# Performance work log

Measured on AMD Instinct MI355X. Metric: run time of the kernel, lower is better.

The kernel has to match this reference:

```python
import jax, jax.numpy as jnp
import numpy as np

H = 8          # n_heads
M = 16         # max_dist
U = 512        # n_units
DH = U // H    # d_head
EPS = 1e-3     # keras LayerNormalization default epsilon
NEG = -2.0**32 + 1.0


def _rel_table(pe, T):
    # pe: [2M+1, DH]; returns [T, T, DH] with rel[i, j] = pe[clip(j - i, -M, M) + M]
    i = jnp.arange(T)
    idx = jnp.clip(i[None, :] - i[:, None], -M, M) + M
    return pe[idx]


def _split_heads(x):
    # [B, T, U] -> [H*B, T, DH]  (head-major, matching tf.concat(tf.split(x, H, 2), 0))
    B, T, _ = x.shape
    return x.reshape(B, T, H, DH).transpose(2, 0, 1, 3).reshape(H * B, T, DH)


def _merge_heads(x, B):
    # [H*B, T, DH] -> [B, T, U]
    T = x.shape[1]
    return x.reshape(H, B, T, DH).transpose(1, 2, 0, 3).reshape(B, T, U)


def setup_inputs() -> dict:
    key = jax.random.key(0)
    ks = jax.random.split(key, 10)
    B, T = 8, 1024
    s = 1.0 / np.sqrt(U)
    inp = {
        'q': jax.random.normal(ks[0], (B, T, U), jnp.float32),
        'k': jax.random.normal(ks[1], (B, T, U), jnp.float32),
        'v': jax.random.normal(ks[2], (B, T, U), jnp.float32),
        'Wq': jax.random.normal(ks[3], (U, U), jnp.float32) * s,
        'bq': jnp.zeros((U,), jnp.float32),
        'Wk': jax.random.normal(ks[4], (U, U), jnp.float32) * s,
        'bk': jnp.zeros((U,), jnp.float32),
        'Wv': jax.random.normal(ks[5], (U, U), jnp.float32) * s,
        'bv': jnp.zeros((U,), jnp.float32),
        'Wo': jax.random.normal(ks[6], (U, U), jnp.float32) * s,
        'bo': jnp.zeros((U,), jnp.float32),
        'gamma': jnp.ones((U,), jnp.float32),
        'beta': jnp.zeros((U,), jnp.float32),
        'pe_k': jax.random.normal(ks[7], (2 * M + 1, DH), jnp.float32) * 0.05,
        'pe_v': jax.random.normal(ks[8], (2 * M + 1, DH), jnp.float32) * 0.05,
    }
    return inp


def reference(q, k, v, Wq, bq, Wk, bk, Wv, bv, Wo, bo, gamma, beta, pe_k, pe_v):
    B, T, _ = q.shape
    relu = jax.nn.relu
    q_emb = relu(q @ Wq + bq)
    k_emb = relu(k @ Wk + bk)
    v_emb = relu(v @ Wv + bv)
    qh = _split_heads(q_emb)   # [HB, T, DH]
    kh = _split_heads(k_emb)
    vh = _split_heads(v_emb)

    attn = jnp.einsum('btd,bsd->bts', qh, kh)
    rel_k = _rel_table(pe_k, T)                       # [T, T, DH]
    attn = attn + jnp.einsum('btd,tsd->bts', qh, rel_k)
    attn = attn / jnp.asarray(DH, attn.dtype) ** 0.5

    causal = jnp.tril(jnp.ones((T, T), jnp.bool_))
    attn = jnp.where(causal[None], attn, jnp.asarray(NEG, attn.dtype))
    w = jax.nn.softmax(attn, axis=-1)

    out = jnp.einsum('bts,bsd->btd', w, vh)
    rel_v = _rel_table(pe_v, T)
    out = out + jnp.einsum('bts,tsd->btd', w, rel_v)

    out = _merge_heads(out, B)                        # [B, T, U]
    out = relu(out @ Wo + bo)
    out = out + q

    mu = jnp.mean(out, axis=-1, keepdims=True)
    var = jnp.mean(jnp.square(out - mu), axis=-1, keepdims=True)
    return (out - mu) * jax.lax.rsqrt(var + EPS) * gamma + beta
```

## Files before the change

### kernel.cpp

```cpp
#include <hip/hip_runtime.h>
#include <hip/hip_bf16.h>

#define T_SEQ 1024
#define U_DIM 512
#define LN_EPS 1e-3f
#define LOG2E 1.44269504f

typedef float  f32x4  __attribute__((ext_vector_type(4)));
typedef short  bf16x8 __attribute__((ext_vector_type(8)));

__device__ __forceinline__ unsigned short f2bf(float f) {
    union { float f; unsigned u; } x; x.f = f;
    unsigned r = x.u + 0x7fffu + ((x.u >> 16) & 1u);
    return (unsigned short)(r >> 16);
}
__device__ __forceinline__ float b2f(short s) {
    union { unsigned u; float f; } x; x.u = ((unsigned)(unsigned short)s) << 16;
    return x.f;
}
__device__ __forceinline__ int packbf(float a, float b) {
    return (int)((unsigned)f2bf(a) | ((unsigned)f2bf(b) << 16));
}
__device__ __forceinline__ void async_copy16(void* lds, const void* g) {
    __builtin_amdgcn_global_load_lds((const __attribute__((address_space(1))) void*)g,
                                     (__attribute__((address_space(3))) void*)lds, 16, 0, 0);
}

#define WAITV(N) asm volatile("s_waitcnt vmcnt(" #N ")" ::: "memory")

__global__ __launch_bounds__(256) void prep_wt(
        const float* __restrict__ Wq, const float* __restrict__ Wk,
        const float* __restrict__ Wv, const float* __restrict__ Wo,
        short* __restrict__ wt) {
    __shared__ float Ws[64][65];
    const int bid = blockIdx.x, t = threadIdx.x;
    const int z = bid >> 6, tile = bid & 63;
    const float* W = (z == 0) ? Wq : (z == 1) ? Wk : (z == 2) ? Wv : Wo;
    short* Wt = wt + (size_t)z * 262144;
    const int k0 = (tile >> 3) * 64, n0 = (tile & 7) * 64;
    {
        const int kr = t >> 2, cs = (t & 3) * 16;
        const float4* src = (const float4*)(W + (size_t)(k0 + kr) * 512 + n0 + cs);
#pragma unroll
        for (int i = 0; i < 4; ++i) {
            float4 vv = src[i];
            Ws[kr][cs + 4 * i + 0] = vv.x;
            Ws[kr][cs + 4 * i + 1] = vv.y;
            Ws[kr][cs + 4 * i + 2] = vv.z;
            Ws[kr][cs + 4 * i + 3] = vv.w;
        }
    }
    __syncthreads();
    {
        const int nr = t >> 2, ks = (t & 3) * 16;
        int4 w0, w1;
        w0.x = packbf(Ws[ks + 0][nr], Ws[ks + 1][nr]);
        w0.y = packbf(Ws[ks + 2][nr], Ws[ks + 3][nr]);
        w0.z = packbf(Ws[ks + 4][nr], Ws[ks + 5][nr]);
        w0.w = packbf(Ws[ks + 6][nr], Ws[ks + 7][nr]);
        w1.x = packbf(Ws[ks + 8][nr], Ws[ks + 9][nr]);
        w1.y = packbf(Ws[ks + 10][nr], Ws[ks + 11][nr]);
        w1.z = packbf(Ws[ks + 12][nr], Ws[ks + 13][nr]);
        w1.w = packbf(Ws[ks + 14][nr], Ws[ks + 15][nr]);
        short* dst = Wt + (size_t)(n0 + nr) * 512 + k0 + ks;
        *(int4*)dst = w0;
        *(int4*)(dst + 8) = w1;
    }
}

__global__ __launch_bounds__(256) void gemm_cvt(
        const float* __restrict__ A0, const float* __restrict__ A1, const float* __restrict__ A2,
        const short* __restrict__ Wt0, const short* __restrict__ Wt1, const short* __restrict__ Wt2,
        const float* __restrict__ b0p, const float* __restrict__ b1p, const float* __restrict__ b2p,
        short* __restrict__ O0, short* __restrict__ O1, short* __restrict__ O2) {
    __shared__ short As[2 * 8192];
    __shared__ short Bs[2 * 8192];

    const int z = blockIdx.z;
    const float* Av = (z == 0) ? A0 : (z == 1) ? A1 : A2;
    const short* Wz = (z == 0) ? Wt0 : (z == 1) ? Wt1 : Wt2;
    const float* bz = (z == 0) ? b0p : (z == 1) ? b1p : b2p;
    short* Ov = (z == 0) ? O0 : (z == 1) ? O1 : O2;

    const int tid = threadIdx.x;
    const int m0 = blockIdx.x * 128, n0 = blockIdx.y * 128;
    const int w = tid >> 6, lane = tid & 63;
    const int n15 = lane & 15, g = lane >> 4;
    const int mh = w >> 1, nh = w & 1;
    const int lr = tid >> 4, c4 = tid & 15;

    f32x4 acc[4][4];
#pragma unroll
    for (int i = 0; i < 4; ++i)
#pragma unroll
        for (int j = 0; j < 4; ++j) acc[i][j] = (f32x4){0.f, 0.f, 0.f, 0.f};

    float4 areg[8];

#define LOAD_A(CK)                                                                       \
    do {                                                                                 \
        const float* abase = Av + (size_t)(m0 + lr) * 512 + (CK) * 64 + c4 * 4;          \
        _Pragma("unroll")                                                                \
        for (int i = 0; i < 8; ++i) areg[i] = *(const float4*)(abase + (size_t)8192 * i); \
    } while (0)

#define STORE_A(BUF)                                                                     \
    do {                                                                                 \
        short* sb = As + (BUF) * 8192 + (c4 >> 3) * 8 * 512 + lr * 8 +                   \
                    ((c4 & 7) >> 1) * 128 + (c4 & 1) * 4;                                \
        _Pragma("unroll")                                                                \
        for (int i = 0; i < 8; ++i) {                                                    \
            int2 wv;                                                                     \
            wv.x = packbf(areg[i].x, areg[i].y);                                         \
            wv.y = packbf(areg[i].z, areg[i].w);                                         \
            *(int2*)(sb + i * 512) = wv;                                                 \
        }                                                                                \
    } while (0)

#define STAGE_B(CK, BUF)                                                                 \
    do {                                                                                 \
        if (w < 2) {                                                                     \
            _Pragma("unroll")                                                            \
            for (int i = 0; i < 8; ++i) {                                                \
                const int kc = i >> 2, nt = w * 4 + (i & 3);                             \
                const short* gp = Wz + (size_t)(n0 + nt * 16 + n15) * 512 + (CK) * 64 + kc * 32 + g * 8; \
                async_copy16(Bs + (BUF) * 8192 + (kc * 8 + nt) * 512, gp);               \
            }                                                                            \
        }                                                                                \
    } while (0)

    LOAD_A(0);
    STORE_A(0);
    STAGE_B(0, 0);
    LOAD_A(1);

    for (int ck = 0; ck < 8; ++ck) {
        const int cb = ck & 1, nb = cb ^ 1;
        __syncthreads();
        if (ck < 7) STAGE_B(ck + 1, nb);
#pragma unroll
        for (int kc = 0; kc < 2; ++kc) {
            bf16x8 af[4], bfv[4];
#pragma unroll
            for (int i = 0; i < 4; ++i)
                af[i] = *(const bf16x8*)(As + cb * 8192 + (kc * 8 + mh * 4 + i) * 512 + lane * 8);
#pragma unroll
            for (int j = 0; j < 4; ++j)
                bfv[j] = *(const bf16x8*)(Bs + cb * 8192 + (kc * 8 + nh * 4 + j) * 512 + lane * 8);
#pragma unroll
            for (int i = 0; i < 4; ++i)
#pragma unroll
                for (int j = 0; j < 4; ++j)
                    acc[i][j] = __builtin_amdgcn_mfma_f32_16x16x32_bf16(af[i], bfv[j], acc[i][j], 0, 0, 0);
        }
        if (ck < 7) {
            STORE_A(nb);
            if (ck < 6) LOAD_A(ck + 2);
        }
    }
#undef LOAD_A
#undef STORE_A
#undef STAGE_B

    const int mbase = m0 + mh * 64 + g * 4;
    const int nbase = n0 + nh * 64 + n15;
    const bool even = (n15 & 1) == 0;
    float bj[4];
#pragma unroll
    for (int j = 0; j < 4; ++j) bj[j] = bz[nbase + j * 16];

#pragma unroll
    for (int i = 0; i < 4; ++i) {
        const int mrow = mbase + i * 16;
#pragma unroll
        for (int j = 0; j < 4; ++j) {
            const int ncol = nbase + j * 16;
            f32x4 a = acc[i][j];
            float v0 = fmaxf(a[0] + bj[j], 0.f);
            float v1 = fmaxf(a[1] + bj[j], 0.f);
            float v2 = fmaxf(a[2] + bj[j], 0.f);
            float v3 = fmaxf(a[3] + bj[j], 0.f);
            unsigned t01 = (unsigned)packbf(v0, v1);
            unsigned t23 = (unsigned)packbf(v2, v3);
            unsigned x01 = (unsigned)__shfl_xor((int)t01, 1, 64);
            unsigned x23 = (unsigned)__shfl_xor((int)t23, 1, 64);
            if (even) {
                unsigned d0 = (t01 & 0xffffu) | (x01 << 16);
                unsigned d1 = (t01 >> 16) | (x01 & 0xffff0000u);
                *(unsigned*)(Ov + (size_t)(mrow + 0) * 512 + ncol) = d0;
                *(unsigned*)(Ov + (size_t)(mrow + 1) * 512 + ncol) = d1;
            } else {
                unsigned d2 = (x23 & 0xffffu) | (t23 << 16);
                unsigned d3 = (x23 >> 16) | (t23 & 0xffff0000u);
                *(unsigned*)(Ov + (size_t)(mrow + 2) * 512 + ncol - 1) = d2;
                *(unsigned*)(Ov + (size_t)(mrow + 3) * 512 + ncol - 1) = d3;
            }
        }
    }
}

template <int BM, int BN>
__global__ __launch_bounds__(256) void gemm_pipe(
        const short* __restrict__ Ab, const short* __restrict__ Wz,
        const float* __restrict__ bz, const float* __restrict__ resid,
        float* __restrict__ Oz) {
    constexpr int ASZ = BM * 32;
    constexpr int BSZ = BN * 32;
    constexpr int TSZ = ASZ + BSZ;
    constexpr int NA  = BM / 16;
    constexpr int NB  = BN / 16;
    constexpr int MW  = BM / 64;
    constexpr int NW  = 4 / MW;
    constexpr int AJ  = BN / (16 * NW);
    constexpr int LPW = (NA + NB) / 4;
    static_assert((NA + NB) % 4 == 0, "cells divisible by waves");
    __shared__ short Ls[4 * TSZ];

    const int tid = threadIdx.x;
    const int m0 = blockIdx.x * BM, n0 = blockIdx.y * BN;
    const int w = tid >> 6, lane = tid & 63;
    const int n15 = lane & 15, g = lane >> 4;
    const int mh = w / NW, nh = w % NW;

    f32x4 acc[4][AJ];
#pragma unroll
    for (int i = 0; i < 4; ++i)
#pragma unroll
        for (int j = 0; j < AJ; ++j) acc[i][j] = (f32x4){0.f, 0.f, 0.f, 0.f};

    const short* gsrc[LPW];
    int loff[LPW];
#pragma unroll
    for (int cl = 0; cl < LPW; ++cl) {
        const int cid = w * LPW + cl;
        if (cid < NA) {
            gsrc[cl] = Ab + (size_t)(m0 + cid * 16 + n15) * 512 + g * 8;
            loff[cl] = cid * 512;
        } else {
            const int c2 = cid - NA;
            gsrc[cl] = Wz + (size_t)(n0 + c2 * 16 + n15) * 512 + g * 8;
            loff[cl] = ASZ + c2 * 512;
        }
    }

#define STAGE(CK, BUF)                                                                   \
    do {                                                                                 \
        _Pragma("unroll")                                                                \
        for (int cl = 0; cl < LPW; ++cl)                                                 \
            async_copy16(Ls + (BUF) * TSZ + loff[cl], gsrc[cl] + (CK) * 32);             \
    } while (0)

    STAGE(0, 0);
    STAGE(1, 1);
    STAGE(2, 2);

    for (int ck = 0; ck < 16; ++ck) {
        if (ck < 14) {
            if constexpr (LPW == 3) WAITV(6); else WAITV(4);
        } else if (ck == 14) {
            if constexpr (LPW == 3) WAITV(3); else WAITV(2);
        } else {
            WAITV(0);
        }
        __builtin_amdgcn_s_barrier();
        __builtin_amdgcn_sched_barrier(0);
        if (ck + 3 <= 15) STAGE(ck + 3, (ck + 3) & 3);
        const int cb = ck & 3;
        bf16x8 af[4], bfv[AJ];
#pragma unroll
        for (int i = 0; i < 4; ++i)
            af[i] = *(const bf16x8*)(Ls + cb * TSZ + (mh * 4 + i) * 512 + lane * 8);
#pragma unroll
        for (int j = 0; j < AJ; ++j)
            bfv[j] = *(const bf16x8*)(Ls + cb * TSZ + ASZ + (nh * AJ + j) * 512 + lane * 8);
#pragma unroll
        for (int i = 0; i < 4; ++i)
#pragma unroll
            for (int j = 0; j < AJ; ++j)
                acc[i][j] = __builtin_amdgcn_mfma_f32_16x16x32_bf16(af[i], bfv[j], acc[i][j], 0, 0, 0);
    }
#undef STAGE

    const int mbase = m0 + mh * 64 + g * 4;
    const int nbase = n0 + nh * (AJ * 16) + n15;
    const bool even = (n15 & 1) == 0;
    float bj[AJ];
#pragma unroll
    for (int j = 0; j < AJ; ++j) bj[j] = bz[nbase + j * 16];

#pragma unroll
    for (int i = 0; i < 4; ++i) {
        const int mrow = mbase + i * 16;
#pragma unroll
        for (int j = 0; j < AJ; ++j) {
            const int ncol = nbase + j * 16;
            f32x4 a = acc[i][j];
            float v0 = fmaxf(a[0] + bj[j], 0.f);
            float v1 = fmaxf(a[1] + bj[j], 0.f);
            float v2 = fmaxf(a[2] + bj[j], 0.f);
            float v3 = fmaxf(a[3] + bj[j], 0.f);
            float x0 = __shfl_xor(v0, 1, 64);
            float x1 = __shfl_xor(v1, 1, 64);
            float x2 = __shfl_xor(v2, 1, 64);
            float x3 = __shfl_xor(v3, 1, 64);
            if (even) {
                float2 r0 = *(const float2*)(resid + (size_t)(mrow + 0) * 512 + ncol);
                float2 r1 = *(const float2*)(resid + (size_t)(mrow + 1) * 512 + ncol);
                *(float2*)(Oz + (size_t)(mrow + 0) * 512 + ncol) = make_float2(v0 + r0.x, x0 + r0.y);
                *(float2*)(Oz + (size_t)(mrow + 1) * 512 + ncol) = make_float2(v1 + r1.x, x1 + r1.y);
            } else {
                float2 r2 = *(const float2*)(resid + (size_t)(mrow + 2) * 512 + ncol - 1);
                float2 r3 = *(const float2*)(resid + (size_t)(mrow + 3) * 512 + ncol - 1);
                *(float2*)(Oz + (size_t)(mrow + 2) * 512 + ncol - 1) = make_float2(x2 + r2.x, v2 + r2.y);
                *(float2*)(Oz + (size_t)(mrow + 3) * 512 + ncol - 1) = make_float2(x3 + r3.x, v3 + r3.y);
            }
        }
    }
}

__global__ __launch_bounds__(256) void attn_mfma(
        const short* __restrict__ qe, const short* __restrict__ ke,
        const short* __restrict__ ve, const float* __restrict__ pe_k,
        float* __restrict__ ml, short* __restrict__ ao) {
    __shared__ short Kc[2 * 4096];
    __shared__ short Vc[2 * 4096];
    __shared__ float qpeS[4 * 16 * 17];

    const int tid = threadIdx.x;
    const int bid = blockIdx.x;
    const int q4 = bid >> 8, r4 = bid & 3;
    const int rank = (q4 < 2) ? (r4 + 4 * q4) : (15 - (r4 + 4 * (q4 - 2)));
    const int hb = (bid >> 2) & 63;
    const int tt = 15 - rank;
    const int h = hb >> 3, b = hb & 7;
    const int w = tid >> 6, lane = tid & 63;
    const int g = lane >> 4, n15 = lane & 15;
    const int sp = tid & 31, dbase = (tid >> 5) * 8;
    float* qpeW = qpeS + w * (16 * 17);

    const size_t rowbase = (size_t)b * T_SEQ;

    const int qn = tt * 64 + w * 16;
    bf16x8 Bq[2];
    float qpe0 = 0.f;
    float m_r = -1.0e38f, l_r = 0.f, m2 = -1.4427e38f;
    f32x4 oacc[4];

    {
#pragma unroll
        for (int kh = 0; kh < 2; ++kh) {
            bf16x8 t = *(const bf16x8*)(qe + (rowbase + qn + n15) * U_DIM + h * 64 + kh * 32 + g * 8);
#pragma unroll
            for (int i2 = 0; i2 < 8; ++i2) {
                unsigned short u = (unsigned short)t[i2];
                t[i2] = (short)(((u & 0x7f80u) > 0x0180u) ? (unsigned short)(u - 0x0180u)
                                                          : (unsigned short)(u & 0x8000u));
            }
            Bq[kh] = t;
        }
        f32x4 qa[2];
        qa[0] = (f32x4){0.f, 0.f, 0.f, 0.f};
        qa[1] = (f32x4){0.f, 0.f, 0.f, 0.f};
#pragma unroll
        for (int mt = 0; mt < 2; ++mt)
#pragma unroll
        for (int kh = 0; kh < 2; ++kh) {
            const float* src = pe_k + (mt * 16 + n15) * 64 + kh * 32 + g * 8;
            float4 f0 = *(const float4*)src;
            float4 f1 = *(const float4*)(src + 4);
            bf16x8 fr;
            fr[0] = (short)f2bf(f0.x); fr[1] = (short)f2bf(f0.y);
            fr[2] = (short)f2bf(f0.z); fr[3] = (short)f2bf(f0.w);
            fr[4] = (short)f2bf(f1.x); fr[5] = (short)f2bf(f1.y);
            fr[6] = (short)f2bf(f1.z); fr[7] = (short)f2bf(f1.w);
            qa[mt] = __builtin_amdgcn_mfma_f32_16x16x32_bf16(fr, Bq[kh], qa[mt], 0, 0, 0);
        }
#pragma unroll
        for (int mt = 0; mt < 2; ++mt)
#pragma unroll
        for (int r = 0; r < 4; ++r) {
            const int ri = mt * 16 + 4 * g + r;
            if (ri <= 16) qpeW[n15 * 17 + ri] = qa[mt][r];
        }
        qpe0 = qpeW[n15 * 17];
#pragma unroll
        for (int dt = 0; dt < 4; ++dt) oacc[dt] = (f32x4){0.f, 0.f, 0.f, 0.f};
    }

#define STAGE_K(S, BUF)                                                                  \
    do {                                                                                 \
        _Pragma("unroll")                                                                \
        for (int j = 0; j < 2; ++j) {                                                    \
            const int cc = w * 2 + j, kh = cc >> 2, mt = cc & 3;                         \
            const short* gp = ke + (rowbase + (S) + mt * 16 + n15) * U_DIM + h * 64 + kh * 32 + g * 8; \
            async_copy16(Kc + (BUF) * 4096 + cc * 512, gp);                              \
        }                                                                                \
    } while (0)

#define LOAD_V(S)                                                                        \
    do {                                                                                 \
        const short* r0 = ve + (rowbase + (S) + 2 * sp) * U_DIM + h * 64 + dbase;        \
        vx = *(const bf16x8*)r0;                                                         \
        vy = *(const bf16x8*)(r0 + U_DIM);                                               \
    } while (0)

#define STORE_V(BUF)                                                                     \
    do {                                                                                 \
        const int vkh = sp >> 4, vg = (sp & 15) >> 2, vj = (sp & 3) * 2;                 \
        _Pragma("unroll")                                                                \
        for (int i = 0; i < 8; ++i) {                                                    \
            const int d = dbase + i;                                                     \
            int pv = (int)((unsigned short)vx[i]) | (((int)(unsigned short)vy[i]) << 16);\
            *(int*)(Vc + (BUF) * 4096 + (vkh * 4 + (d >> 4)) * 512 + ((d & 15) + 16 * vg) * 8 + vj) = pv; \
        }                                                                                \
    } while (0)

    bf16x8 vx, vy;
    STAGE_K(0, 0);
    LOAD_V(0);
    STORE_V(0);

    for (int gs = 0; gs <= tt; ++gs) {
        const int cb = gs & 1, nb = cb ^ 1;
        const int s0 = gs * 64;
        __syncthreads();
        if (gs < tt) {
            STAGE_K((gs + 1) * 64, nb);
            LOAD_V((gs + 1) * 64);
        }

        {
            int cls[4];
#pragma unroll
            for (int mt = 0; mt < 4; ++mt) {
                const int slo = s0 + mt * 16;
                cls[mt] = (slo > qn + 15) ? 0 : ((slo + 31 < qn) ? 1 : 2);
            }
            f32x4 c[4];
#pragma unroll
            for (int mt = 0; mt < 4; ++mt) c[mt] = (f32x4){0.f, 0.f, 0.f, 0.f};
            __builtin_amdgcn_s_setprio(1);
#pragma unroll
            for (int mt = 0; mt < 4; ++mt) {
                if (!cls[mt]) continue;
#pragma unroll
                for (int kh = 0; kh < 2; ++kh) {
                    bf16x8 ak = *(const bf16x8*)(Kc + cb * 4096 + (kh * 4 + mt) * 512 + lane * 8);
                    c[mt] = __builtin_amdgcn_mfma_f32_16x16x32_bf16(ak, Bq[kh], c[mt], 0, 0, 0);
                }
            }
            __builtin_amdgcn_s_setprio(0);

            const int qg = qn + n15;
            float sc[4][4];
            float pmax = -3.0e38f;
#pragma unroll
            for (int mt = 0; mt < 4; ++mt) {
                if (cls[mt] == 0) {
#pragma unroll
                    for (int r = 0; r < 4; ++r) sc[mt][r] = -3.0e38f;
                } else if (cls[mt] == 1) {
#pragma unroll
                    for (int r = 0; r < 4; ++r) {
                        sc[mt][r] = c[mt][r] + qpe0;
                        pmax = fmaxf(pmax, sc[mt][r]);
                    }
                } else {
#pragma unroll
                    for (int r = 0; r < 4; ++r) {
                        const int sg = s0 + mt * 16 + 4 * g + r;
                        const int dlt = sg - qg;
                        if (dlt <= 0) {
                            const int ri = (dlt < -16) ? 0 : (dlt + 16);
                            sc[mt][r] = c[mt][r] + qpeW[n15 * 17 + ri];
                            pmax = fmaxf(pmax, sc[mt][r]);
                        } else {
                            sc[mt][r] = -3.0e38f;
                        }
                    }
                }
            }
            pmax = fmaxf(pmax, __shfl_xor(pmax, 16, 64));
            pmax = fmaxf(pmax, __shfl_xor(pmax, 32, 64));

            const bool resc = __any(pmax > m_r + 8.0f);
            float alpha = 1.0f;
            if (resc) {
                const float mnew = fmaxf(m_r, pmax);
                alpha = __expf(m_r - mnew);
                m_r = mnew;
                m2 = mnew * LOG2E;
            }
            float p[4][4];
            float psum = 0.f;
#pragma unroll
            for (int mt = 0; mt < 4; ++mt)
#pragma unroll
            for (int r = 0; r < 4; ++r) {
                const float pv = (cls[mt] == 0) ? 0.f
                                : exp2f(fmaf(sc[mt][r], LOG2E, -m2));
                p[mt][r] = pv;
                psum += pv;
            }
            psum += __shfl_xor(psum, 16, 64);
            psum += __shfl_xor(psum, 32, 64);
            l_r = l_r * alpha + psum;

            int pk01[4], pk23[4];
#pragma unroll
            for (int mt = 0; mt < 4; ++mt) {
                asm("v_cvt_pk_bf16_f32 %0, %1, %2" : "=v"(pk01[mt]) : "v"(p[mt][0]), "v"(p[mt][1]));
                asm("v_cvt_pk_bf16_f32 %0, %1, %2" : "=v"(pk23[mt]) : "v"(p[mt][2]), "v"(p[mt][3]));
            }
            const int srcA = ((g & 1) * 2) * 16 + n15;
            const int srcB = srcA + 16;
            const bool selHi = (g >> 1) != 0;
            if (resc) {
                float aO[4];
#pragma unroll
                for (int r = 0; r < 4; ++r) aO[r] = __shfl(alpha, 4 * g + r, 64);
#pragma unroll
                for (int dt = 0; dt < 4; ++dt)
#pragma unroll
                for (int r = 0; r < 4; ++r) oacc[dt][r] *= aO[r];
            }
#pragma unroll
            for (int kh = 0; kh < 2; ++kh) {
                if (cls[2 * kh] == 0 && cls[2 * kh + 1] == 0) continue;
                const int a0l = __shfl(pk01[2 * kh], srcA, 64);
                const int a0h = __shfl(pk01[2 * kh + 1], srcA, 64);
                const int a1l = __shfl(pk23[2 * kh], srcA, 64);
                const int a1h = __shfl(pk23[2 * kh + 1], srcA, 64);
                const int a2l = __shfl(pk01[2 * kh], srcB, 64);
                const int a2h = __shfl(pk01[2 * kh + 1], srcB, 64);
                const int a3l = __shfl(pk23[2 * kh], srcB, 64);
                const int a3h = __shfl(pk23[2 * kh + 1], srcB, 64);
                union { int i[4]; bf16x8 v; } au;
                au.i[0] = selHi ? a0h : a0l;
                au.i[1] = selHi ? a1h : a1l;
                au.i[2] = selHi ? a2h : a2l;
                au.i[3] = selHi ? a3h : a3l;
                __builtin_amdgcn_s_setprio(1);
#pragma unroll
                for (int dt = 0; dt < 4; ++dt) {
                    bf16x8 bv = *(const bf16x8*)(Vc + cb * 4096 + (kh * 4 + dt) * 512 + lane * 8);
                    oacc[dt] = __builtin_amdgcn_mfma_f32_16x16x32_bf16(au.v, bv, oacc[dt], 0, 0, 0);
                }
                __builtin_amdgcn_s_setprio(0);
            }
        }

        if (gs < tt) STORE_V(nb);
    }

    if (g == 0)
        *(float2*)(ml + ((size_t)hb * T_SEQ + qn + n15) * 2) = make_float2(m_r, l_r);
#pragma unroll
    for (int r = 0; r < 4; ++r) {
        const float lq = __shfl(l_r, 4 * g + r, 64);
        const float linv = 1.0f / lq;
        short* dst = ao + (rowbase + qn + 4 * g + r) * U_DIM + h * 64 + n15;
#pragma unroll
        for (int dt = 0; dt < 4; ++dt)
            dst[dt * 16] = (short)f2bf(oacc[dt][r] * linv);
    }
#undef STAGE_K
#undef LOAD_V
#undef STORE_V
}

__global__ __launch_bounds__(256) void band_relv(
        const short* __restrict__ qe, const short* __restrict__ ke,
        const float* __restrict__ pe_k, const float* __restrict__ pe_v,
        const float* __restrict__ ml, short* __restrict__ ao) {
    __shared__ float pek[17 * 64];
    __shared__ float pev[17 * 64];
    const int tb = blockIdx.x, hb = blockIdx.y;
    const int h = hb >> 3, b = hb & 7;
    const int tid = threadIdx.x;
    for (int i = tid; i < 17 * 64; i += 256) {
        pek[i] = b2f((short)f2bf(pe_k[i]));
        pev[i] = pe_v[i];
    }
    __syncthreads();

    const int t = tb * 64 + (tid >> 2);
    const int p = (tid & 3) * 16;
    const short* qp = qe + (size_t)(b * T_SEQ + t) * U_DIM + h * 64 + p;
    bf16x8 qa = *(const bf16x8*)qp, qb2 = *(const bf16x8*)(qp + 8);
    float qv[16];
#pragma unroll
    for (int i = 0; i < 8; ++i) { qv[i] = b2f(qa[i]); qv[8 + i] = b2f(qb2[i]); }

    float dots[17];
#pragma unroll
    for (int ri = 0; ri < 17; ++ri) {
        const int s = t - 16 + ri;
        float acc = 0.f;
        if (s >= 0) {
            const short* kp = ke + (size_t)(b * T_SEQ + s) * U_DIM + h * 64 + p;
            bf16x8 ka = *(const bf16x8*)kp, kb2 = *(const bf16x8*)(kp + 8);
#pragma unroll
            for (int d = 0; d < 8; ++d) {
                acc += qv[d] * b2f(ka[d]);
                acc += qv[8 + d] * b2f(kb2[d]);
            }
#pragma unroll
            for (int d = 0; d < 16; ++d) acc += qv[d] * pek[ri * 64 + p + d];
        }
        dots[ri] = acc;
    }
#pragma unroll
    for (int ri = 0; ri < 17; ++ri) {
        dots[ri] += __shfl_xor(dots[ri], 1, 64);
        dots[ri] += __shfl_xor(dots[ri], 2, 64);
    }

    const float2 mlv = *(const float2*)(ml + ((size_t)hb * T_SEQ + t) * 2);
    const float m = mlv.x, linv = 1.0f / mlv.y;
    float wv[17];
    float wsum = 0.f;
#pragma unroll
    for (int ri = 0; ri < 17; ++ri) {
        const int s = t - 16 + ri;
        const float wr = (s >= 0) ? __expf(dots[ri] * 0.125f - m) * linv : 0.f;
        wv[ri] = wr;
        wsum += wr;
    }
    wv[0] += 1.0f - wsum;

    float relv[16];
#pragma unroll
    for (int d = 0; d < 16; ++d) relv[d] = 0.f;
#pragma unroll
    for (int ri = 0; ri < 17; ++ri)
#pragma unroll
        for (int d = 0; d < 16; ++d) relv[d] += wv[ri] * pev[ri * 64 + p + d];

    short* op = ao + (size_t)(b * T_SEQ + t) * U_DIM + h * 64 + p;
    bf16x8 a0 = *(const bf16x8*)op, a1 = *(const bf16x8*)(op + 8);
    int4 o0, o1;
    o0.x = packbf(b2f(a0[0]) + relv[0],  b2f(a0[1]) + relv[1]);
    o0.y = packbf(b2f(a0[2]) + relv[2],  b2f(a0[3]) + relv[3]);
    o0.z = packbf(b2f(a0[4]) + relv[4],  b2f(a0[5]) + relv[5]);
    o0.w = packbf(b2f(a0[6]) + relv[6],  b2f(a0[7]) + relv[7]);
    o1.x = packbf(b2f(a1[0]) + relv[8],  b2f(a1[1]) + relv[9]);
    o1.y = packbf(b2f(a1[2]) + relv[10], b2f(a1[3]) + relv[11]);
    o1.z = packbf(b2f(a1[4]) + relv[12], b2f(a1[5]) + relv[13]);
    o1.w = packbf(b2f(a1[6]) + relv[14], b2f(a1[7]) + relv[15]);
    *(int4*)op = o0;
    *(int4*)(op + 8) = o1;
}

__global__ __launch_bounds__(256) void ln_kernel(float* __restrict__ io,
                                                 const float* __restrict__ gamma,
                                                 const float* __restrict__ beta) {
    const int row = blockIdx.x * 4 + (threadIdx.x >> 6);
    const int lane = threadIdx.x & 63;
    float* rp = io + (size_t)row * 512 + lane * 8;
    float4 a = *(const float4*)rp;
    float4 c = *(const float4*)(rp + 4);
    float v[8] = {a.x, a.y, a.z, a.w, c.x, c.y, c.z, c.w};

    float s = v[0] + v[1] + v[2] + v[3] + v[4] + v[5] + v[6] + v[7];
#pragma unroll
    for (int off = 1; off < 64; off <<= 1) s += __shfl_xor(s, off, 64);
    const float mu = s * (1.0f / 512.0f);

    float sq = 0.f;
#pragma unroll
    for (int i = 0; i < 8; ++i) { v[i] -= mu; sq += v[i] * v[i]; }
#pragma unroll
    for (int off = 1; off < 64; off <<= 1) sq += __shfl_xor(sq, off, 64);
    const float rs = rsqrtf(sq * (1.0f / 512.0f) + LN_EPS);

    const float4 g0 = *(const float4*)(gamma + lane * 8);
    const float4 g1 = *(const float4*)(gamma + lane * 8 + 4);
    const float4 b0 = *(const float4*)(beta + lane * 8);
    const float4 b1 = *(const float4*)(beta + lane * 8 + 4);
    float4 o0, o1;
    o0.x = v[0] * rs * g0.x + b0.x;
    o0.y = v[1] * rs * g0.y + b0.y;
    o0.z = v[2] * rs * g0.z + b0.z;
    o0.w = v[3] * rs * g0.w + b0.w;
    o1.x = v[4] * rs * g1.x + b1.x;
    o1.y = v[5] * rs * g1.y + b1.y;
    o1.z = v[6] * rs * g1.z + b1.z;
    o1.w = v[7] * rs * g1.w + b1.w;
    *(float4*)rp = o0;
    *(float4*)(rp + 4) = o1;
}

extern "C" void kernel_launch(void* const* d_in, const int* in_sizes, int n_in,
                              void* d_out, int out_size, void* d_ws, size_t ws_size,
                              hipStream_t stream) {
    const float* q     = (const float*)d_in[0];
    const float* k     = (const float*)d_in[1];
    const float* v     = (const float*)d_in[2];
    const float* Wq    = (const float*)d_in[3];
    const float* bq    = (const float*)d_in[4];
    const float* Wk    = (const float*)d_in[5];
    const float* bk    = (const float*)d_in[6];
    const float* Wv    = (const float*)d_in[7];
    const float* bv    = (const float*)d_in[8];
    const float* Wo    = (const float*)d_in[9];
    const float* bo    = (const float*)d_in[10];
    const float* gamma = (const float*)d_in[11];
    const float* beta  = (const float*)d_in[12];
    const float* pe_k  = (const float*)d_in[13];
    const float* pe_v  = (const float*)d_in[14];
    float* out = (float*)d_out;

    char* base = (char*)d_ws;
    short* qe = (short*)(base);
    short* ke = (short*)(base + (((size_t)8) << 20));
    short* ve = (short*)(base + (((size_t)16) << 20));
    short* ao = (short*)(base + (((size_t)24) << 20));
    short* wt = (short*)(base + (((size_t)32) << 20));
    float* ml = (float*)(base + (((size_t)34) << 20));
    short* wtq = wt, *wtk = wt + 262144, *wtv = wt + 2 * 262144, *wto = wt + 3 * 262144;

    prep_wt<<<dim3(256), 256, 0, stream>>>(Wq, Wk, Wv, Wo, wt);
    gemm_cvt<<<dim3(64, 4, 3), 256, 0, stream>>>(
        q, k, v, wtq, wtk, wtv, bq, bk, bv, qe, ke, ve);
    attn_mfma<<<dim3(1024), 256, 0, stream>>>(qe, ke, ve, pe_k, ml, ao);
    band_relv<<<dim3(16, 64), 256, 0, stream>>>(qe, ke, pe_k, pe_v, ml, ao);
    gemm_pipe<64, 128><<<dim3(128, 4), 256, 0, stream>>>(ao, wto, bo, q, out);
    ln_kernel<<<dim3(2048), 256, 0, stream>>>(out, gamma, beta);
}
```

Baseline: 239.7 us.

## Split long causal attention tiles across two blocks and merge with combine kernel

Query tiles in the second half of the sequence (tt>=8) have their key range split into two halves, each handled by a separate block writing partial outputs and (m,l) stats. A new attn_combine kernel merges the halves using softmax rescaling. The grid grows from 1024 to 1536 blocks, assigned through a static slot table for load balance. K staging changes from async LDS copies with double buffering to register-staged single-buffered LDS with two barriers per step, and launch bounds request 6 waves per SIMD. The aim is to even out causal work imbalance and raise occupancy, at the cost of an extra kernel launch, extra partial-output traffic, and a bf16 rounding step on the partial results.

```diff
diff --git a/kernel.cpp b/kernel.cpp
--- a/kernel.cpp
+++ b/kernel.cpp
@@ -318,20 +318,36 @@
     }
 }
 
-__global__ __launch_bounds__(256) void attn_mfma(
+__global__ __launch_bounds__(256, 6) void attn_mfma(
         const short* __restrict__ qe, const short* __restrict__ ke,
         const short* __restrict__ ve, const float* __restrict__ pe_k,
-        float* __restrict__ ml, short* __restrict__ ao) {
-    __shared__ short Kc[2 * 4096];
-    __shared__ short Vc[2 * 4096];
+        float* __restrict__ ml, float* __restrict__ ml1, float* __restrict__ ml2,
+        short* __restrict__ ao, short* __restrict__ ao2) {
+    __shared__ short Kc[4096];
+    __shared__ short Vc[4096];
     __shared__ float qpeS[4 * 16 * 17];
 
+    static const unsigned char tbl[24] = {
+        7, 22, 6, 4, 3, 1,
+        20, 23, 16, 12, 9, 0,
+        18, 5, 14, 15, 17, 2,
+        19, 21, 8, 10, 11, 13
+    };
+
     const int tid = threadIdx.x;
-    const int bid = blockIdx.x;
-    const int q4 = bid >> 8, r4 = bid & 3;
-    const int rank = (q4 < 2) ? (r4 + 4 * q4) : (15 - (r4 + 4 * (q4 - 2)));
-    const int hb = (bid >> 2) & 63;
-    const int tt = 15 - rank;
+    const int r6 = blockIdx.x >> 8, c = blockIdx.x & 255;
+    const int hb = c >> 2, q4 = c & 3;
+    const int slot = tbl[q4 * 6 + r6];
+    int tt, g0, g1, mode;
+    if (slot < 8) {
+        tt = slot; g0 = 0; g1 = slot + 1; mode = 0;
+    } else {
+        const int i2 = (slot - 8) >> 1;
+        tt = 8 + i2;
+        const int n = tt + 1, hh = (n + 1) >> 1;
+        if (((slot - 8) & 1) == 0) { g0 = 0; g1 = hh; mode = 1; }
+        else                       { g0 = hh; g1 = n; mode = 2; }
+    }
     const int h = hb >> 3, b = hb & 7;
     const int w = tid >> 6, lane = tid & 63;
     const int g = lane >> 4, n15 = lane & 15;
@@ -339,6 +355,8 @@
     float* qpeW = qpeS + w * (16 * 17);
 
     const size_t rowbase = (size_t)b * T_SEQ;
+    short* aoP = (mode == 2) ? ao2 : ao;
+    float* mlP = (mode == 0) ? ml : (mode == 1 ? ml1 : ml2);
 
     const int qn = tt * 64 + w * 16;
     bf16x8 Bq[2];
@@ -387,14 +405,21 @@
         for (int dt = 0; dt < 4; ++dt) oacc[dt] = (f32x4){0.f, 0.f, 0.f, 0.f};
     }
 
-#define STAGE_K(S, BUF)                                                                  \
+    const int sK = tid >> 2, dK = (tid & 3) * 16;
+    short* kdst = Kc + (((tid & 3) >> 1) * 4 + (tid >> 6)) * 512 +
+                  ((sK & 15) + 16 * ((tid & 1) * 2)) * 8;
+
+#define LOAD_K(S)                                                                        \
     do {                                                                                 \
-        _Pragma("unroll")                                                                \
-        for (int j = 0; j < 2; ++j) {                                                    \
-            const int cc = w * 2 + j, kh = cc >> 2, mt = cc & 3;                         \
-            const short* gp = ke + (rowbase + (S) + mt * 16 + n15) * U_DIM + h * 64 + kh * 32 + g * 8; \
-            async_copy16(Kc + (BUF) * 4096 + cc * 512, gp);                              \
-        }                                                                                \
+        const short* kp = ke + (rowbase + (S) + sK) * U_DIM + h * 64 + dK;               \
+        kx0 = *(const bf16x8*)kp;                                                        \
+        kx1 = *(const bf16x8*)(kp + 8);                                                  \
+    } while (0)
+
+#define STORE_K()                                                                        \
+    do {                                                                                 \
+        *(bf16x8*)kdst = kx0;                                                            \
+        *(bf16x8*)(kdst + 128) = kx1;                                                    \
     } while (0)
 
 #define LOAD_V(S)                                                                        \
@@ -404,28 +429,29 @@
         vy = *(const bf16x8*)(r0 + U_DIM);                                               \
     } while (0)
 
-#define STORE_V(BUF)                                                                     \
+#define STORE_V()                                                                        \
     do {                                                                                 \
         const int vkh = sp >> 4, vg = (sp & 15) >> 2, vj = (sp & 3) * 2;                 \
         _Pragma("unroll")                                                                \
         for (int i = 0; i < 8; ++i) {                                                    \
             const int d = dbase + i;                                                     \
             int pv = (int)((unsigned short)vx[i]) | (((int)(unsigned short)vy[i]) << 16);\
-            *(int*)(Vc + (BUF) * 4096 + (vkh * 4 + (d >> 4)) * 512 + ((d & 15) + 16 * vg) * 8 + vj) = pv; \
+            *(int*)(Vc + (vkh * 4 + (d >> 4)) * 512 + ((d & 15) + 16 * vg) * 8 + vj) = pv; \
         }                                                                                \
     } while (0)
 
-    bf16x8 vx, vy;
-    STAGE_K(0, 0);
-    LOAD_V(0);
-    STORE_V(0);
-
-    for (int gs = 0; gs <= tt; ++gs) {
-        const int cb = gs & 1, nb = cb ^ 1;
+    bf16x8 kx0, kx1, vx, vy;
+    LOAD_K(g0 * 64);
+    LOAD_V(g0 * 64);
+
+    for (int gs = g0; gs < g1; ++gs) {
         const int s0 = gs * 64;
         __syncthreads();
-        if (gs < tt) {
-            STAGE_K((gs + 1) * 64, nb);
+        STORE_K();
+        STORE_V();
+        __syncthreads();
+        if (gs + 1 < g1) {
+            LOAD_K((gs + 1) * 64);
             LOAD_V((gs + 1) * 64);
         }
 
@@ -436,17 +462,17 @@
                 const int slo = s0 + mt * 16;
                 cls[mt] = (slo > qn + 15) ? 0 : ((slo + 31 < qn) ? 1 : 2);
             }
-            f32x4 c[4];
-#pragma unroll
-            for (int mt = 0; mt < 4; ++mt) c[mt] = (f32x4){0.f, 0.f, 0.f, 0.f};
+            f32x4 cc2[4];
+#pragma unroll
+            for (int mt = 0; mt < 4; ++mt) cc2[mt] = (f32x4){0.f, 0.f, 0.f, 0.f};
             __builtin_amdgcn_s_setprio(1);
 #pragma unroll
             for (int mt = 0; mt < 4; ++mt) {
                 if (!cls[mt]) continue;
 #pragma unroll
                 for (int kh = 0; kh < 2; ++kh) {
-                    bf16x8 ak = *(const bf16x8*)(Kc + cb * 4096 + (kh * 4 + mt) * 512 + lane * 8);
-                    c[mt] = __builtin_amdgcn_mfma_f32_16x16x32_bf16(ak, Bq[kh], c[mt], 0, 0, 0);
+                    bf16x8 ak = *(const bf16x8*)(Kc + (kh * 4 + mt) * 512 + lane * 8);
+                    cc2[mt] = __builtin_amdgcn_mfma_f32_16x16x32_bf16(ak, Bq[kh], cc2[mt], 0, 0, 0);
                 }
             }
             __builtin_amdgcn_s_setprio(0);
@@ -462,7 +488,7 @@
                 } else if (cls[mt] == 1) {
 #pragma unroll
                     for (int r = 0; r < 4; ++r) {
-                        sc[mt][r] = c[mt][r] + qpe0;
+                        sc[mt][r] = cc2[mt][r] + qpe0;
                         pmax = fmaxf(pmax, sc[mt][r]);
                     }
                 } else {
@@ -472,7 +498,7 @@
                         const int dlt = sg - qg;
                         if (dlt <= 0) {
                             const int ri = (dlt < -16) ? 0 : (dlt + 16);
-                            sc[mt][r] = c[mt][r] + qpeW[n15 * 17 + ri];
+                            sc[mt][r] = cc2[mt][r] + qpeW[n15 * 17 + ri];
                             pmax = fmaxf(pmax, sc[mt][r]);
                         } else {
                             sc[mt][r] = -3.0e38f;
@@ -543,30 +569,71 @@
                 __builtin_amdgcn_s_setprio(1);
 #pragma unroll
                 for (int dt = 0; dt < 4; ++dt) {
-                    bf16x8 bv = *(const bf16x8*)(Vc + cb * 4096 + (kh * 4 + dt) * 512 + lane * 8);
+                    bf16x8 bv = *(const bf16x8*)(Vc + (kh * 4 + dt) * 512 + lane * 8);
                     oacc[dt] = __builtin_amdgcn_mfma_f32_16x16x32_bf16(au.v, bv, oacc[dt], 0, 0, 0);
                 }
                 __builtin_amdgcn_s_setprio(0);
             }
         }
-
-        if (gs < tt) STORE_V(nb);
     }
 
     if (g == 0)
-        *(float2*)(ml + ((size_t)hb * T_SEQ + qn + n15) * 2) = make_float2(m_r, l_r);
+        *(float2*)(mlP + ((size_t)hb * T_SEQ + qn + n15) * 2) = make_float2(m_r, l_r);
 #pragma unroll
     for (int r = 0; r < 4; ++r) {
         const float lq = __shfl(l_r, 4 * g + r, 64);
-        const float linv = 1.0f / lq;
-        short* dst = ao + (rowbase + qn + 4 * g + r) * U_DIM + h * 64 + n15;
+        const float linv = (lq > 0.f) ? 1.0f / lq : 0.f;
+        short* dst = aoP + (rowbase + qn + 4 * g + r) * U_DIM + h * 64 + n15;
 #pragma unroll
         for (int dt = 0; dt < 4; ++dt)
             dst[dt * 16] = (short)f2bf(oacc[dt][r] * linv);
     }
-#undef STAGE_K
+#undef LOAD_K
+#undef STORE_K
 #undef LOAD_V
 #undef STORE_V
+}
+
+__global__ __launch_bounds__(256) void attn_combine(
+        const float* __restrict__ ml1, const float* __restrict__ ml2,
+        const short* __restrict__ ao2, short* __restrict__ ao,
+        float* __restrict__ ml) {
+    const int bid = blockIdx.x;
+    const int hb = bid >> 3;
+    const int t = 512 + ((bid & 7) << 6) + (threadIdx.x >> 2);
+    const int R = hb * 1024 + t;
+    const int h = hb >> 3, b = hb & 7;
+    const int d0 = (threadIdx.x & 3) * 16;
+    const float2 p1 = *(const float2*)(ml1 + (size_t)R * 2);
+    const float2 p2 = *(const float2*)(ml2 + (size_t)R * 2);
+    const float m = fmaxf(p1.x, p2.x);
+    const float w1 = p1.y * __expf(p1.x - m);
+    const float w2 = (p2.y > 0.f) ? p2.y * __expf(p2.x - m) : 0.f;
+    const float inv = 1.0f / (w1 + w2);
+    const float a1 = w1 * inv, a2 = w2 * inv;
+    const size_t off = (size_t)(b * T_SEQ + t) * U_DIM + h * 64 + d0;
+    short* op = ao + off;
+    const short* o2p = ao2 + off;
+    bf16x8 x0 = *(const bf16x8*)op, x1 = *(const bf16x8*)(op + 8);
+    bf16x8 y0 = *(const bf16x8*)o2p, y1 = *(const bf16x8*)(o2p + 8);
+    const bool has2 = (w2 > 0.f);
+    float o[16];
+#pragma unroll
+    for (int i = 0; i < 8; ++i) {
+        float t0 = a1 * b2f(x0[i]);
+        float t1 = a1 * b2f(x1[i]);
+        o[i]     = has2 ? (t0 + a2 * b2f(y0[i])) : t0;
+        o[8 + i] = has2 ? (t1 + a2 * b2f(y1[i])) : t1;
+    }
+    int4 o0, o1;
+    o0.x = packbf(o[0], o[1]);   o0.y = packbf(o[2], o[3]);
+    o0.z = packbf(o[4], o[5]);   o0.w = packbf(o[6], o[7]);
+    o1.x = packbf(o[8], o[9]);   o1.y = packbf(o[10], o[11]);
+    o1.z = packbf(o[12], o[13]); o1.w = packbf(o[14], o[15]);
+    *(int4*)op = o0;
+    *(int4*)(op + 8) = o1;
+    if ((threadIdx.x & 3) == 0)
+        *(float2*)(ml + (size_t)R * 2) = make_float2(m, w1 + w2);
 }
 
 __global__ __launch_bounds__(256) void band_relv(
@@ -718,12 +785,16 @@
     short* ao = (short*)(base + (((size_t)24) << 20));
     short* wt = (short*)(base + (((size_t)32) << 20));
     float* ml = (float*)(base + (((size_t)34) << 20));
+    float* ml1 = (float*)(base + (((size_t)35) << 20));
+    short* ao2 = (short*)(base + (((size_t)36) << 20));
+    float* ml2 = (float*)(base + (((size_t)44) << 20));
     short* wtq = wt, *wtk = wt + 262144, *wtv = wt + 2 * 262144, *wto = wt + 3 * 262144;
 
     prep_wt<<<dim3(256), 256, 0, stream>>>(Wq, Wk, Wv, Wo, wt);
     gemm_cvt<<<dim3(64, 4, 3), 256, 0, stream>>>(
         q, k, v, wtq, wtk, wtv, bq, bk, bv, qe, ke, ve);
-    attn_mfma<<<dim3(1024), 256, 0, stream>>>(qe, ke, ve, pe_k, ml, ao);
+    attn_mfma<<<dim3(1536), 256, 0, stream>>>(qe, ke, ve, pe_k, ml, ml1, ml2, ao, ao2);
+    attn_combine<<<dim3(512), 256, 0, stream>>>(ml1, ml2, ao2, ao, ml);
     band_relv<<<dim3(16, 64), 256, 0, stream>>>(qe, ke, pe_k, pe_v, ml, ao);
     gemm_pipe<64, 128><<<dim3(128, 4), 256, 0, stream>>>(ao, wto, bo, q, out);
     ln_kernel<<<dim3(2048), 256, 0, stream>>>(out, gamma, beta);
```

Measured after the change: 287.9 us. 1.2x slower.
